# Performance work log

Hardware: AMD Instinct MI355X
Metric: run time of the kernel (lower is better)

Reference implementation:

```python
import jax, jax.numpy as jnp
import numpy as np

BS, N, F_IN, H, F_OUT = 4, 2048, 128, 4, 64


def setup_inputs() -> dict:
    key = jax.random.key(0)
    k1, k2, k3, k4, k5 = jax.random.split(key, 5)
    x = jax.random.normal(k1, (BS, N, F_IN), dtype=jnp.float32)
    adj = jax.random.randint(k2, (BS, N, N), 0, 2).astype(bool)
    # guarantee self-loops so no softmax row is all -inf
    adj = jnp.logical_or(adj, jnp.eye(N, dtype=bool)[None])
    # xavier-uniform-ish scales
    w = jax.random.uniform(k3, (H, F_IN, F_OUT), dtype=jnp.float32,
                           minval=-1.0, maxval=1.0) * np.sqrt(6.0 / (F_IN + F_OUT))
    a_src = jax.random.uniform(k4, (H, F_OUT, 1), dtype=jnp.float32,
                               minval=-1.0, maxval=1.0) * np.sqrt(6.0 / (F_OUT + 1))
    a_dst = jax.random.uniform(k5, (H, F_OUT, 1), dtype=jnp.float32,
                               minval=-1.0, maxval=1.0) * np.sqrt(6.0 / (F_OUT + 1))
    bias = jnp.zeros((F_OUT,), dtype=jnp.float32)
    return {"x": x, "adj": adj, "w": w, "a_src": a_src, "a_dst": a_dst, "bias": bias}


def reference(x, adj, w, a_src, a_dst, bias):
    bs, n = x.shape[:2]
    # h_prime: [bs, H, n, F_OUT]
    h = jnp.einsum('bnf,hfo->bhno', x, w)
    th = jnp.tanh(h)
    s_src = jnp.einsum('bhno,ho->bhn', th, a_src[..., 0])  # [bs,H,n]
    s_dst = jnp.einsum('bhno,ho->bhn', th, a_dst[..., 0])  # [bs,H,n]
    # attn[b,h,i,j] = src[b,h,i] + dst[b,h,j]
    attn = s_src[..., :, None] + s_dst[..., None, :]
    attn = jnp.where(attn >= 0, attn, 0.2 * attn)  # leaky_relu(0.2)
    attn = jnp.where(adj[:, None], attn, -jnp.inf)  # mask = ~adj
    p = jax.nn.softmax(attn, axis=-1)  # dropout is identity at eval
    out = jnp.einsum('bhij,bhjo->bhio', p, h) + bias  # [bs,H,n,F_OUT]
    # torch .view(bs, n, -1) on contiguous [bs,H,n,F_OUT]: raw reshape
    return out.reshape(bs, n, -1)
```

## Files before the change

kernel.cpp:

```cpp
#include <hip/hip_runtime.h>
#include <hip/hip_fp16.h>

#define NN   2048
#define FIN  128
#define FOUT 64
#define LOG2E 1.44269504088896f

using f16x8 = __attribute__((ext_vector_type(8))) _Float16;
using f16x4 = __attribute__((ext_vector_type(4))) _Float16;
using f16x2 = __attribute__((ext_vector_type(2))) _Float16;
using f32x4 = __attribute__((ext_vector_type(4))) float;
using i32x4 = __attribute__((ext_vector_type(4))) int;

__device__ inline float fast_exp2(float x) {
#if __has_builtin(__builtin_amdgcn_exp2f)
    return __builtin_amdgcn_exp2f(x);
#else
    return exp2f(x);
#endif
}
__device__ inline float fast_rcp(float x) {
#if __has_builtin(__builtin_amdgcn_rcpf)
    return __builtin_amdgcn_rcpf(x);
#else
    return 1.0f / x;
#endif
}
__device__ inline float fast_tanh(float x) {
    float e = fast_exp2(2.0f * LOG2E * x);
    return 1.0f - 2.0f * fast_rcp(e + 1.0f);
}
__device__ inline unsigned cvt2h(float a, float b) {
    return __builtin_bit_cast(unsigned, __builtin_amdgcn_cvt_pkrtz(a, b));
}
__device__ inline f16x2 pkmax(f16x2 a, f16x2 b) {
#if __has_builtin(__builtin_elementwise_max)
    return __builtin_elementwise_max(a, b);
#else
    f16x2 r; r[0] = a[0] > b[0] ? a[0] : b[0]; r[1] = a[1] > b[1] ? a[1] : b[1];
    return r;
#endif
}
__device__ inline unsigned bmask(unsigned wb, int p) {
    unsigned lo = (unsigned)(-(int)((wb >> (2 * p)) & 1u));
    unsigned hi = (unsigned)(-(int)((wb >> (2 * p + 1)) & 1u));
    return (hi & 0xFFFF0000u) | (lo & 0x0000FFFFu);
}


__global__ __launch_bounds__(256) void k1_proj(
    const float* __restrict__ x, const float* __restrict__ w,
    const float* __restrict__ a_src, const float* __restrict__ a_dst,
    const int* __restrict__ adj,
    _Float16* __restrict__ h16B, float* __restrict__ ssrc, float* __restrict__ sdst,
    unsigned int* __restrict__ adjbits)
{
    __shared__ __align__(16) _Float16 xf[8192];
    __shared__ __align__(16) _Float16 wf[8192];

    const int t    = threadIdx.x;
    const int bx   = blockIdx.x;
    const int bh   = bx >> 5;
    const int tile = bx & 31;
    const int b    = bh >> 2;
    const int h    = bh & 3;
    const int n0   = tile * 64;
    const int wv   = t >> 6;
    const int lane = t & 63;
    const int m    = lane & 15;
    const int g    = lane >> 4;

    {
        const int o  = t & 63;
        const int kc = t >> 6;
        const float* wcol = w + h * FIN * FOUT + o;
        _Float16* dst = wf + ((kc * 4 + (o >> 4)) * 512) + (o & 15) * 8;
#pragma unroll
        for (int hi = 0; hi < 4; ++hi) {
            unsigned u0 = cvt2h(wcol[(kc * 32 + hi * 8 + 0) * FOUT],
                                wcol[(kc * 32 + hi * 8 + 1) * FOUT]);
            unsigned u1 = cvt2h(wcol[(kc * 32 + hi * 8 + 2) * FOUT],
                                wcol[(kc * 32 + hi * 8 + 3) * FOUT]);
            unsigned u2 = cvt2h(wcol[(kc * 32 + hi * 8 + 4) * FOUT],
                                wcol[(kc * 32 + hi * 8 + 5) * FOUT]);
            unsigned u3 = cvt2h(wcol[(kc * 32 + hi * 8 + 6) * FOUT],
                                wcol[(kc * 32 + hi * 8 + 7) * FOUT]);
            *(uint4*)(dst + hi * 128) = uint4{u0, u1, u2, u3};
        }
    }
    {
        const int r  = t >> 2;
        const int kc = t & 3;
        const float* xr = x + ((size_t)(b * NN + n0 + r)) * FIN + kc * 32;
        _Float16* dst = xf + ((r >> 4) * 16 + kc * 4) * 128 + (r & 15) * 8;
#pragma unroll
        for (int g2 = 0; g2 < 4; ++g2) {
            f32x4 va = *(const f32x4*)(xr + g2 * 8);
            f32x4 vb = *(const f32x4*)(xr + g2 * 8 + 4);
            *(uint4*)(dst + g2 * 128) = uint4{cvt2h(va[0], va[1]), cvt2h(va[2], va[3]),
                                              cvt2h(vb[0], vb[1]), cvt2h(vb[2], vb[3])};
        }
    }
    __syncthreads();

    const int rg = wv;
    f32x4 acc0 = {0,0,0,0}, acc1 = {0,0,0,0}, acc2 = {0,0,0,0}, acc3 = {0,0,0,0};
#pragma unroll
    for (int kc = 0; kc < 4; ++kc) {
        f16x8 av = *(const f16x8*)(xf + (rg * 16 + kc * 4 + g) * 128 + m * 8);
        const _Float16* wb_ = wf + kc * 4 * 512 + lane * 8;
        acc0 = __builtin_amdgcn_mfma_f32_16x16x32_f16(av, *(const f16x8*)(wb_), acc0, 0, 0, 0);
        acc1 = __builtin_amdgcn_mfma_f32_16x16x32_f16(av, *(const f16x8*)(wb_ + 512), acc1, 0, 0, 0);
        acc2 = __builtin_amdgcn_mfma_f32_16x16x32_f16(av, *(const f16x8*)(wb_ + 1024), acc2, 0, 0, 0);
        acc3 = __builtin_amdgcn_mfma_f32_16x16x32_f16(av, *(const f16x8*)(wb_ + 1536), acc3, 0, 0, 0);
    }

    float s1r[4] = {0,0,0,0}, s2r[4] = {0,0,0,0};
    const int jg = n0 + rg * 16 + g * 4;
#define PROC(accX, ot)  do {                                                    \
        float asv = a_src[h * FOUT + (ot) * 16 + m];                            \
        float adv = a_dst[h * FOUT + (ot) * 16 + m];                            \
        _Pragma("unroll")                                                       \
        for (int r = 0; r < 4; ++r) {                                           \
            float th = fast_tanh(accX[r]);                                      \
            s1r[r] += th * asv;                                                 \
            s2r[r] += th * adv;                                                 \
        }                                                                       \
        unsigned u0 = cvt2h(accX[0], accX[1]);                                  \
        unsigned u1 = cvt2h(accX[2], accX[3]);                                  \
        int off = bh * 131072 + (jg >> 5) * 2048 + (ot) * 512                   \
                + (((jg >> 3) & 3) * 16 + m) * 8 + (jg & 7);                    \
        *(uint2*)(h16B + off) = uint2{u0, u1};                                  \
    } while (0)
    PROC(acc0, 0); PROC(acc1, 1); PROC(acc2, 2); PROC(acc3, 3);
#undef PROC
#pragma unroll
    for (int msk = 1; msk <= 8; msk <<= 1) {
#pragma unroll
        for (int r = 0; r < 4; ++r) {
            s1r[r] += __shfl_xor(s1r[r], msk);
            s2r[r] += __shfl_xor(s2r[r], msk);
        }
    }
    if (m == 0) {
#pragma unroll
        for (int r = 0; r < 4; ++r) {
            ssrc[bh * NN + jg + r] = s1r[r] * LOG2E;
            sdst[bh * NN + jg + r] = s2r[r] * LOG2E;
        }
    }

    {
        const int  frow0 = bx * 16;
        const int* asrc  = adj + (size_t)frow0 * NN;
#pragma unroll
        for (int w4 = 0; w4 < 4; ++w4) {
            int widx  = t + 256 * w4;
            int row_l = widx >> 6;
            int wc    = widx & 63;
            const i32x4* p = (const i32x4*)(asrc + (size_t)row_l * NN + wc * 32);
            unsigned int wbits = 0;
#pragma unroll
            for (int k = 0; k < 8; ++k) {
                i32x4 v = p[k];
                wbits |= (unsigned int)(v[0] & 1) << (4 * k);
                wbits |= (unsigned int)(v[1] & 1) << (4 * k + 1);
                wbits |= (unsigned int)(v[2] & 1) << (4 * k + 2);
                wbits |= (unsigned int)(v[3] & 1) << (4 * k + 3);
            }
            adjbits[(size_t)(frow0 + row_l) * 64 + wc] = wbits;
        }
    }
}

__global__ __launch_bounds__(512, 6) void k2_attn(
    const unsigned int* __restrict__ adjbits,
    const _Float16* __restrict__ h16B,
    const float* __restrict__ ssrc, const float* __restrict__ sdst,
    const float* __restrict__ bias, float* __restrict__ out)
{
    __shared__ __align__(16) char smem[42016];
    _Float16*     Bf     = (_Float16*)smem;
    unsigned int* adjw   = (unsigned int*)(smem + 16384);
    _Float16*     E1h    = (_Float16*)(smem + 33792);
    _Float16*     E2h    = (_Float16*)(smem + 37888);
    float*        redmax = (float*)(smem + 41984);
    float*        comb   = (float*)smem;

    const int t    = threadIdx.x;
    const int wv   = t >> 6;
    const int lane = t & 63;
    const int bh   = blockIdx.x >> 5;
    const int i0   = (blockIdx.x & 31) << 6;
    const int b    = bh >> 2;
    const int rg   = wv >> 1;
    const int par  = wv & 1;
    const int m    = lane & 15;
    const int g    = lane >> 4;

    const _Float16* Bsrc = h16B + bh * 131072;

#define STAGE(bufi_, s_)                                                        \
    __builtin_amdgcn_global_load_lds(                                           \
        (const __attribute__((address_space(1))) unsigned int*)(Bsrc + (s_) * 4096 + t * 8), \
        (__attribute__((address_space(3))) unsigned int*)(Bf + (bufi_) * 4096 + t * 8), \
        16, 0, 0)

    STAGE(0, 0);
    {
        const uint4* asrc = (const uint4*)(adjbits + ((size_t)b * NN + i0) * 64);
#pragma unroll
        for (int k = 0; k < 2; ++k) {
            int idx = t + 512 * k;
            uint4 v = asrc[idx];
            *(uint4*)(adjw + (idx >> 4) * 68 + (idx & 15) * 4) = v;
        }
    }
    {
        f32x4 dv = *(const f32x4*)(sdst + bh * NN + t * 4);
        *(uint2*)(E1h + t * 4) = uint2{cvt2h(fast_exp2(dv[0]), fast_exp2(dv[1])),
                                       cvt2h(fast_exp2(dv[2]), fast_exp2(dv[3]))};
        *(uint2*)(E2h + t * 4) = uint2{cvt2h(fast_exp2(0.2f * dv[0]), fast_exp2(0.2f * dv[1])),
                                       cvt2h(fast_exp2(0.2f * dv[2]), fast_exp2(0.2f * dv[3]))};
        float dm = fmaxf(fmaxf(dv[0], dv[1]), fmaxf(dv[2], dv[3]));
#pragma unroll
        for (int msk = 1; msk <= 32; msk <<= 1) dm = fmaxf(dm, __shfl_xor(dm, msk));
        if (lane == 0) redmax[wv] = dm;
    }
    asm volatile("s_waitcnt vmcnt(0)" ::: "memory");
    __syncthreads();

    float D = redmax[0];
#pragma unroll
    for (int k = 1; k < 8; ++k) D = fmaxf(D, redmax[k]);

    const int row = i0 + rg * 16 + m;
    const float sA = ssrc[bh * NN + row];
    float c = sA + D; c = fmaxf(c, 0.2f * c);
    const float K1f = fast_exp2(sA - c);
    const float K2f = fast_exp2(fmaf(0.2f, sA, -c));
    f16x2 K1h2; { _Float16 q = (_Float16)K1f; K1h2[0] = q; K1h2[1] = q; }
    f16x2 K2h2; { _Float16 q = (_Float16)K2f; K2h2[0] = q; K2h2[1] = q; }

    f32x4 acc0 = {0,0,0,0}, acc1 = {0,0,0,0}, acc2 = {0,0,0,0}, acc3 = {0,0,0,0};
    f32x4 accz = {0,0,0,0};
    f16x8 ones;
#pragma unroll
    for (int i = 0; i < 8; ++i) ones[i] = (_Float16)1.0f;

    const int arow68 = (rg * 16 + m) * 68;

    union afu { f16x8 v; f16x2 p[4]; unsigned u[4]; };

#define EGEN(af_, s_) do {                                                      \
        const int ci_ = 2 * (s_) + par;                                         \
        unsigned wb_ = adjw[arow68 + ci_] >> (8 * g);                           \
        afu E1u_, E2u_;                                                         \
        E1u_.v = *(const f16x8*)(E1h + ci_ * 32 + 8 * g);                       \
        E2u_.v = *(const f16x8*)(E2h + ci_ * 32 + 8 * g);                       \
        _Pragma("unroll")                                                       \
        for (int p = 0; p < 4; ++p) {                                           \
            f16x2 v1 = K1h2 * E1u_.p[p];                                        \
            f16x2 v2 = K2h2 * E2u_.p[p];                                        \
            af_.u[p] = __builtin_bit_cast(unsigned, pkmax(v1, v2)) & bmask(wb_, p); \
        }                                                                       \
    } while (0)

    afu afc;
    EGEN(afc, 0);

#pragma unroll
    for (int s = 0; s < 32; ++s) {
        if (s < 31) {
            STAGE((s + 1) & 1, s + 1);
            asm volatile("s_waitcnt vmcnt(1)" ::: "memory");
        } else {
            asm volatile("s_waitcnt vmcnt(0)" ::: "memory");
        }
        __builtin_amdgcn_sched_barrier(0);
        __builtin_amdgcn_s_barrier();

        const _Float16* bb = Bf + (s & 1) * 4096 + par * 2048 + lane * 8;
        f16x8 b0 = *(const f16x8*)(bb);
        f16x8 b1 = *(const f16x8*)(bb + 512);
        f16x8 b2 = *(const f16x8*)(bb + 1024);
        f16x8 b3 = *(const f16x8*)(bb + 1536);

        acc0 = __builtin_amdgcn_mfma_f32_16x16x32_f16(afc.v, b0, acc0, 0, 0, 0);
        acc1 = __builtin_amdgcn_mfma_f32_16x16x32_f16(afc.v, b1, acc1, 0, 0, 0);
        acc2 = __builtin_amdgcn_mfma_f32_16x16x32_f16(afc.v, b2, acc2, 0, 0, 0);
        acc3 = __builtin_amdgcn_mfma_f32_16x16x32_f16(afc.v, b3, acc3, 0, 0, 0);
        accz = __builtin_amdgcn_mfma_f32_16x16x32_f16(afc.v, ones, accz, 0, 0, 0);

        if (s < 31) EGEN(afc, s + 1);

        __builtin_amdgcn_s_barrier();
    }
#undef EGEN
#undef STAGE

    __syncthreads();
    if (par == 1) {
        float* cp = comb + (rg * 64 + lane) * 20;
#pragma unroll
        for (int r = 0; r < 4; ++r) {
            cp[0 + r]  = acc0[r];
            cp[4 + r]  = acc1[r];
            cp[8 + r]  = acc2[r];
            cp[12 + r] = acc3[r];
            cp[16 + r] = accz[r];
        }
    }
    __syncthreads();
    if (par == 0) {
        const float* cp = comb + (rg * 64 + lane) * 20;
        float zs[4];
#pragma unroll
        for (int r = 0; r < 4; ++r) zs[r] = accz[r] + cp[16 + r];
        size_t obase = ((size_t)bh * NN + i0 + rg * 16) * FOUT;
#pragma unroll
        for (int ot = 0; ot < 4; ++ot) {
            float bv = bias[ot * 16 + m];
            f32x4 a = (ot == 0) ? acc0 : (ot == 1) ? acc1 : (ot == 2) ? acc2 : acc3;
#pragma unroll
            for (int r = 0; r < 4; ++r) {
                float v = (a[r] + cp[ot * 4 + r]) / zs[r] + bv;
                out[obase + (size_t)(g * 4 + r) * FOUT + ot * 16 + m] = v;
            }
        }
    }
}

extern "C" void kernel_launch(void* const* d_in, const int* in_sizes, int n_in,
                              void* d_out, int out_size, void* d_ws, size_t ws_size,
                              hipStream_t stream) {
    (void)in_sizes; (void)n_in; (void)out_size; (void)ws_size;
    const float* x     = (const float*)d_in[0];
    const int*   adj   = (const int*)d_in[1];
    const float* w     = (const float*)d_in[2];
    const float* a_src = (const float*)d_in[3];
    const float* a_dst = (const float*)d_in[4];
    const float* bias  = (const float*)d_in[5];
    float*       out   = (float*)d_out;

    _Float16*     h16B    = (_Float16*)d_ws;
    float*        ssrc    = (float*)((char*)d_ws + 4194304);
    float*        sdst    = (float*)((char*)d_ws + 4194304 + 131072);
    unsigned int* adjbits = (unsigned int*)((char*)d_ws + 4718592);

    k1_proj<<<512, 256, 0, stream>>>(x, w, a_src, a_dst, adj, h16B, ssrc, sdst, adjbits);
    k2_attn<<<512, 512, 0, stream>>>(adjbits, h16B, ssrc, sdst, bias, out);
}
```

Measured before the change: 41.03 us.

## Split attention K-dimension across four waves per row group with 1024-thread blocks

Doubles the k2_attn block to 1024 threads so each 16-row group is handled by four waves instead of two, each covering a quarter of the neighbor columns. The loop drops from 32 to 16 stages, each staging twice as much B data into a larger double-buffered LDS region. A two-step LDS tree reduction combines the four partial accumulators. The aim is more waves in flight per CU and shorter serial K loops per wave, at the cost of extra LDS, more barriers and a longer reduction epilogue.

```diff
diff --git a/kernel.cpp b/kernel.cpp
--- a/kernel.cpp
+++ b/kernel.cpp
@@ -173,18 +173,18 @@
     }
 }
 
-__global__ __launch_bounds__(512, 6) void k2_attn(
+__global__ __launch_bounds__(1024, 8) void k2_attn(
     const unsigned int* __restrict__ adjbits,
     const _Float16* __restrict__ h16B,
     const float* __restrict__ ssrc, const float* __restrict__ sdst,
     const float* __restrict__ bias, float* __restrict__ out)
 {
-    __shared__ __align__(16) char smem[42016];
+    __shared__ __align__(16) char smem[58432];
     _Float16*     Bf     = (_Float16*)smem;
-    unsigned int* adjw   = (unsigned int*)(smem + 16384);
-    _Float16*     E1h    = (_Float16*)(smem + 33792);
-    _Float16*     E2h    = (_Float16*)(smem + 37888);
-    float*        redmax = (float*)(smem + 41984);
+    unsigned int* adjw   = (unsigned int*)(smem + 32768);
+    _Float16*     E1h    = (_Float16*)(smem + 50176);
+    _Float16*     E2h    = (_Float16*)(smem + 54272);
+    float*        redmax = (float*)(smem + 58368);
     float*        comb   = (float*)smem;
 
     const int t    = threadIdx.x;
@@ -193,8 +193,8 @@
     const int bh   = blockIdx.x >> 5;
     const int i0   = (blockIdx.x & 31) << 6;
     const int b    = bh >> 2;
-    const int rg   = wv >> 1;
-    const int par  = wv & 1;
+    const int rg   = wv >> 2;
+    const int quad = wv & 3;
     const int m    = lane & 15;
     const int g    = lane >> 4;
 
@@ -202,27 +202,22 @@
 
 #define STAGE(bufi_, s_)                                                        \
     __builtin_amdgcn_global_load_lds(                                           \
-        (const __attribute__((address_space(1))) unsigned int*)(Bsrc + (s_) * 4096 + t * 8), \
-        (__attribute__((address_space(3))) unsigned int*)(Bf + (bufi_) * 4096 + t * 8), \
+        (const __attribute__((address_space(1))) unsigned int*)(Bsrc + (s_) * 8192 + t * 8), \
+        (__attribute__((address_space(3))) unsigned int*)(Bf + (bufi_) * 8192 + t * 8), \
         16, 0, 0)
 
     STAGE(0, 0);
     {
         const uint4* asrc = (const uint4*)(adjbits + ((size_t)b * NN + i0) * 64);
-#pragma unroll
-        for (int k = 0; k < 2; ++k) {
-            int idx = t + 512 * k;
-            uint4 v = asrc[idx];
-            *(uint4*)(adjw + (idx >> 4) * 68 + (idx & 15) * 4) = v;
-        }
-    }
-    {
-        f32x4 dv = *(const f32x4*)(sdst + bh * NN + t * 4);
-        *(uint2*)(E1h + t * 4) = uint2{cvt2h(fast_exp2(dv[0]), fast_exp2(dv[1])),
-                                       cvt2h(fast_exp2(dv[2]), fast_exp2(dv[3]))};
-        *(uint2*)(E2h + t * 4) = uint2{cvt2h(fast_exp2(0.2f * dv[0]), fast_exp2(0.2f * dv[1])),
-                                       cvt2h(fast_exp2(0.2f * dv[2]), fast_exp2(0.2f * dv[3]))};
-        float dm = fmaxf(fmaxf(dv[0], dv[1]), fmaxf(dv[2], dv[3]));
+        uint4 v = asrc[t];
+        *(uint4*)(adjw + (t >> 4) * 68 + (t & 15) * 4) = v;
+    }
+    {
+        const float* sdp = sdst + bh * NN + t * 2;
+        float d0 = sdp[0], d1 = sdp[1];
+        *(unsigned*)(E1h + t * 2) = cvt2h(fast_exp2(d0), fast_exp2(d1));
+        *(unsigned*)(E2h + t * 2) = cvt2h(fast_exp2(0.2f * d0), fast_exp2(0.2f * d1));
+        float dm = fmaxf(d0, d1);
 #pragma unroll
         for (int msk = 1; msk <= 32; msk <<= 1) dm = fmaxf(dm, __shfl_xor(dm, msk));
         if (lane == 0) redmax[wv] = dm;
@@ -232,7 +227,7 @@
 
     float D = redmax[0];
 #pragma unroll
-    for (int k = 1; k < 8; ++k) D = fmaxf(D, redmax[k]);
+    for (int k = 1; k < 16; ++k) D = fmaxf(D, redmax[k]);
 
     const int row = i0 + rg * 16 + m;
     const float sA = ssrc[bh * NN + row];
@@ -253,7 +248,7 @@
     union afu { f16x8 v; f16x2 p[4]; unsigned u[4]; };
 
 #define EGEN(af_, s_) do {                                                      \
-        const int ci_ = 2 * (s_) + par;                                         \
+        const int ci_ = 4 * (s_) + quad;                                        \
         unsigned wb_ = adjw[arow68 + ci_] >> (8 * g);                           \
         afu E1u_, E2u_;                                                         \
         E1u_.v = *(const f16x8*)(E1h + ci_ * 32 + 8 * g);                       \
@@ -270,8 +265,8 @@
     EGEN(afc, 0);
 
 #pragma unroll
-    for (int s = 0; s < 32; ++s) {
-        if (s < 31) {
+    for (int s = 0; s < 16; ++s) {
+        if (s < 15) {
             STAGE((s + 1) & 1, s + 1);
             asm volatile("s_waitcnt vmcnt(1)" ::: "memory");
         } else {
@@ -280,7 +275,7 @@
         __builtin_amdgcn_sched_barrier(0);
         __builtin_amdgcn_s_barrier();
 
-        const _Float16* bb = Bf + (s & 1) * 4096 + par * 2048 + lane * 8;
+        const _Float16* bb = Bf + (s & 1) * 8192 + quad * 2048 + lane * 8;
         f16x8 b0 = *(const f16x8*)(bb);
         f16x8 b1 = *(const f16x8*)(bb + 512);
         f16x8 b2 = *(const f16x8*)(bb + 1024);
@@ -292,7 +287,7 @@
         acc3 = __builtin_amdgcn_mfma_f32_16x16x32_f16(afc.v, b3, acc3, 0, 0, 0);
         accz = __builtin_amdgcn_mfma_f32_16x16x32_f16(afc.v, ones, accz, 0, 0, 0);
 
-        if (s < 31) EGEN(afc, s + 1);
+        if (s < 15) EGEN(afc, s + 1);
 
         __builtin_amdgcn_s_barrier();
     }
@@ -300,8 +295,8 @@
 #undef STAGE
 
     __syncthreads();
-    if (par == 1) {
-        float* cp = comb + (rg * 64 + lane) * 20;
+    if (quad & 1) {
+        float* cp = comb + ((rg * 2 + (quad >> 1)) * 64 + lane) * 20;
 #pragma unroll
         for (int r = 0; r < 4; ++r) {
             cp[0 + r]  = acc0[r];
@@ -312,7 +307,31 @@
         }
     }
     __syncthreads();
-    if (par == 0) {
+    if (!(quad & 1)) {
+        const float* cp = comb + ((rg * 2 + (quad >> 1)) * 64 + lane) * 20;
+#pragma unroll
+        for (int r = 0; r < 4; ++r) {
+            acc0[r] += cp[0 + r];
+            acc1[r] += cp[4 + r];
+            acc2[r] += cp[8 + r];
+            acc3[r] += cp[12 + r];
+            accz[r] += cp[16 + r];
+        }
+    }
+    __syncthreads();
+    if (quad == 2) {
+        float* cp = comb + (rg * 64 + lane) * 20;
+#pragma unroll
+        for (int r = 0; r < 4; ++r) {
+            cp[0 + r]  = acc0[r];
+            cp[4 + r]  = acc1[r];
+            cp[8 + r]  = acc2[r];
+            cp[12 + r] = acc3[r];
+            cp[16 + r] = accz[r];
+        }
+    }
+    __syncthreads();
+    if (quad == 0) {
         const float* cp = comb + (rg * 64 + lane) * 20;
         float zs[4];
 #pragma unroll
@@ -349,5 +368,5 @@
     unsigned int* adjbits = (unsigned int*)((char*)d_ws + 4718592);
 
     k1_proj<<<512, 256, 0, stream>>>(x, w, a_src, a_dst, adj, h16B, ssrc, sdst, adjbits);
-    k2_attn<<<512, 512, 0, stream>>>(adjbits, h16B, ssrc, sdst, bias, out);
-}
+    k2_attn<<<512, 1024, 0, stream>>>(adjbits, h16B, ssrc, sdst, bias, out);
+}
```

New measurement: 42.94 us. 4.7% more time.
